# Optimization experiments

Measured on AMD Instinct MI355X. Metric: run time of the kernel, lower is better.

The kernel has to match this reference:

```python
import jax, jax.numpy as jnp
import numpy as np

N = 8192
HEADS = 2
IN_F = 256
OUT_F = 64
NEG_SLOPE = 0.2
ADJ_DENSITY = 0.01


def setup_inputs() -> dict:
    key = jax.random.key(0)
    k1, k2, k3, k4, k5 = jax.random.split(key, 5)
    x = jax.random.normal(k1, (N, IN_F), dtype=jnp.float32)
    # xavier_uniform with relu gain sqrt(2)
    def xavier(k, shape, fan_in, fan_out):
        gain = float(np.sqrt(2.0))
        limit = gain * float(np.sqrt(6.0 / (fan_in + fan_out)))
        return jax.random.uniform(k, shape, jnp.float32, -limit, limit)
    W = xavier(k2, (HEADS, IN_F, OUT_F), IN_F, OUT_F)
    a_src = xavier(k3, (HEADS, OUT_F, 1), OUT_F, 1)
    a_dst = xavier(k4, (HEADS, OUT_F, 1), OUT_F, 1)
    bias = jnp.zeros((HEADS * OUT_F,), dtype=jnp.float32)
    # sparse 0/1 adjacency used purely as a mask
    adj = (jax.random.uniform(k5, (N, N)) < ADJ_DENSITY).astype(jnp.float32)
    return {"x": x, "W": W, "a_src": a_src, "a_dst": a_dst, "bias": bias, "adj": adj}


def reference(x, W, a_src, a_dst, bias, adj):
    n = x.shape[0]
    # h: (H, N, out)
    h = jnp.einsum('ni,hio->hno', x, W)
    # additive attention logits: e[h,i,j] = src[h,i] + dst[h,j]
    s = jnp.einsum('hno,ho->hn', h, a_src[..., 0])  # (H, N)
    d = jnp.einsum('hno,ho->hn', h, a_dst[..., 0])  # (H, N)
    e = jax.nn.leaky_relu(s[:, :, None] + d[:, None, :], negative_slope=NEG_SLOPE)
    # mask: disallowed where adj + I == 0 (self-loops always kept)
    mask = (adj + jnp.eye(n, dtype=adj.dtype)) == 0  # (N, N)
    e = jnp.where(mask[None], -jnp.inf, e)
    alpha = jax.nn.softmax(e, axis=-1)  # (H, N, N); dropout p=0 -> identity
    out = jnp.einsum('hnm,hmo->hno', alpha, h)  # (H, N, out)
    # concat heads -> (N, H*out), then bias
    out = out.transpose(1, 0, 2).reshape(n, -1) + bias
    return out
```

## Files before the change

kernel.cpp:

```cpp
#include <hip/hip_runtime.h>
#include <hip/hip_bf16.h>
#include <math.h>

#define NN 8192
#define IN_F 256
#define OUT_F 64
#define HEADS 2
#define NEG_SLOPE 0.2f
#define QS 160

__device__ __forceinline__ float lrelu(float v) { return v > 0.0f ? v : NEG_SLOPE * v; }
__device__ __forceinline__ float bf_lo(unsigned u) { return __uint_as_float(u << 16); }
__device__ __forceinline__ float bf_hi(unsigned u) { return __uint_as_float(u & 0xffff0000u); }

__global__ __launch_bounds__(256) void gat_proj(
    const float* __restrict__ x, const float* __restrict__ W,
    const float* __restrict__ a_src, const float* __restrict__ a_dst,
    __hip_bfloat16* __restrict__ hb, float* __restrict__ s_arr,
    float2* __restrict__ d2)
{
    __shared__ float  xs[16 * IN_F];
    __shared__ float2 wch[32 * 64];
    const int tid = threadIdx.x;
    const int r0 = blockIdx.x * 16;

    {
        const float4* xg = (const float4*)(x + (size_t)r0 * IN_F);
        float4* xs4 = (float4*)xs;
#pragma unroll
        for (int v = 0; v < 4; ++v) xs4[v * 256 + tid] = xg[v * 256 + tid];
    }

    const int wave = tid >> 6;
    const int lane = tid & 63;
    const int rbase = wave * 4;

    const float* __restrict__ W0 = W;
    const float* __restrict__ W1 = W + IN_F * OUT_F;

    float acc[4][2] = {{0.f,0.f},{0.f,0.f},{0.f,0.f},{0.f,0.f}};

    for (int kc = 0; kc < 8; ++kc) {
        __syncthreads();
#pragma unroll
        for (int t = 0; t < 8; ++t) {
            const int idx = t * 256 + tid;
            const int kk = idx >> 6, c = idx & 63;
            wch[idx] = make_float2(W0[(kc * 32 + kk) * 64 + c],
                                   W1[(kc * 32 + kk) * 64 + c]);
        }
        __syncthreads();
#pragma unroll 8
        for (int kk = 0; kk < 32; ++kk) {
            const float2 wv = wch[kk * 64 + lane];
#pragma unroll
            for (int r = 0; r < 4; ++r) {
                const float xv = xs[(rbase + r) * IN_F + kc * 32 + kk];
                acc[r][0] += xv * wv.x;
                acc[r][1] += xv * wv.y;
            }
        }
    }

    const float as0 = a_src[lane],         ad0 = a_dst[lane];
    const float as1 = a_src[OUT_F + lane], ad1 = a_dst[OUT_F + lane];

#pragma unroll
    for (int r = 0; r < 4; ++r) {
        const int row = r0 + rbase + r;
        hb[(size_t)row * 128 + lane]      = __float2bfloat16(acc[r][0]);
        hb[(size_t)row * 128 + 64 + lane] = __float2bfloat16(acc[r][1]);
        float v0 = acc[r][0] * as0;
        float v1 = acc[r][0] * ad0;
        float v2 = acc[r][1] * as1;
        float v3 = acc[r][1] * ad1;
#pragma unroll
        for (int off = 32; off; off >>= 1) {
            v0 += __shfl_xor(v0, off);
            v1 += __shfl_xor(v1, off);
            v2 += __shfl_xor(v2, off);
            v3 += __shfl_xor(v3, off);
        }
        if (lane == 0) {
            s_arr[row]      = v0;
            s_arr[NN + row] = v2;
            d2[row] = make_float2(v1, v3);
        }
    }
}

__global__ __launch_bounds__(256, 4) void gat_scan_agg(
    const float* __restrict__ adj, const __hip_bfloat16* __restrict__ hb,
    const float* __restrict__ s_arr, const float2* __restrict__ d2,
    const float* __restrict__ bias, float* __restrict__ out)
{
    __shared__ ushort qs[4][QS];
    __shared__ float2 qw[4][QS];
    const int wave = threadIdx.x >> 6;
    const int lane = threadIdx.x & 63;
    const int i = blockIdx.x * 4 + wave;

    const float s0 = s_arr[i], s1 = s_arr[NN + i];
    const float2 di = d2[i];
    const float M0 = lrelu(s0 + di.x);
    const float M1 = lrelu(s1 + di.y);

    const uint4* __restrict__ arow = (const uint4*)(adj + (size_t)i * NN);
    uint accs[4];
#pragma unroll
    for (int g = 0; g < 4; ++g) {
        uint acc = 0;
#pragma unroll
        for (int b = 0; b < 8; ++b) {
            const uint4 a = arow[(g * 8 + b) * 64 + lane];
            const uint nib = ((a.x >> 23) & 1u) | ((a.y >> 22) & 2u) |
                             ((a.z >> 21) & 4u) | ((a.w >> 20) & 8u);
            acc |= nib << (4 * b);
        }
        accs[g] = acc;
    }

    if (lane == ((i & 255) >> 2)) {
        const int c = i >> 8;
        const int g = c >> 3;
        const uint m = ~(1u << (((c & 7) << 2) | (i & 3)));
        accs[g] &= m;
    }

    const int mycnt = __popc(accs[0]) + __popc(accs[1]) + __popc(accs[2]) + __popc(accs[3]);
    int pre = mycnt;
#pragma unroll
    for (int off = 1; off < 64; off <<= 1) {
        const int v = __shfl_up(pre, off);
        if (lane >= off) pre += v;
    }
    const int base0 = 1 + pre - mycnt;
    int cnt = 1 + __shfl(pre, 63);

    if (lane == 0) qs[wave][0] = (ushort)i;
    {
        int slot = base0;
#pragma unroll
        for (int g = 0; g < 4; ++g) {
            uint w = accs[g];
            while (w) {
                const int idx = __builtin_ctz(w);
                w &= w - 1;
                const int j = g * 2048 + ((idx >> 2) << 8) + (lane << 2) + (idx & 3);
                if (slot < QS - 8) qs[wave][slot] = (ushort)j;
                ++slot;
            }
        }
    }
    cnt = min(cnt, QS - 8);
    if (lane < 7) qs[wave][cnt + lane] = (ushort)i;

    float l0 = 0.f, l1 = 0.f;
    for (int e = lane; e < cnt; e += 64) {
        const int j = qs[wave][e];
        const float2 dv = d2[j];
        const float w0 = __expf(lrelu(s0 + dv.x) - M0);
        const float w1 = __expf(lrelu(s1 + dv.y) - M1);
        qw[wave][e] = make_float2(w0, w1);
        l0 += w0;
        l1 += w1;
    }
    if (lane < 7) qw[wave][cnt + lane] = make_float2(0.f, 0.f);
#pragma unroll
    for (int off = 32; off; off >>= 1) {
        l0 += __shfl_xor(l0, off);
        l1 += __shfl_xor(l1, off);
    }

    const int g = lane >> 4, gl = lane & 15;
    const bool head0 = (gl < 8);
    const uint4* __restrict__ hb4 = (const uint4*)hb;
    float acc[8] = {0.f,0.f,0.f,0.f,0.f,0.f,0.f,0.f};

    const int cntp = (cnt + 7) & ~7;
    for (int e = 0; e < cntp; e += 8) {
        const int ja = qs[wave][e + g];
        const int jb = qs[wave][e + 4 + g];
        const float2 wa2 = qw[wave][e + g];
        const float2 wb2 = qw[wave][e + 4 + g];
        const float wa = head0 ? wa2.x : wa2.y;
        const float wb = head0 ? wb2.x : wb2.y;
        const uint4 va = hb4[(size_t)ja * 16 + gl];
        const uint4 vb = hb4[(size_t)jb * 16 + gl];
        acc[0] += wa * bf_lo(va.x) + wb * bf_lo(vb.x);
        acc[1] += wa * bf_hi(va.x) + wb * bf_hi(vb.x);
        acc[2] += wa * bf_lo(va.y) + wb * bf_lo(vb.y);
        acc[3] += wa * bf_hi(va.y) + wb * bf_hi(vb.y);
        acc[4] += wa * bf_lo(va.z) + wb * bf_lo(vb.z);
        acc[5] += wa * bf_hi(va.z) + wb * bf_hi(vb.z);
        acc[6] += wa * bf_lo(va.w) + wb * bf_lo(vb.w);
        acc[7] += wa * bf_hi(va.w) + wb * bf_hi(vb.w);
    }

#pragma unroll
    for (int off = 16; off <= 32; off <<= 1) {
#pragma unroll
        for (int k = 0; k < 8; ++k) acc[k] += __shfl_xor(acc[k], off);
    }

    const float inv0 = 1.0f / l0;
    const float inv1 = 1.0f / l1;
    if (lane < 16) {
        const float inv = head0 ? inv0 : inv1;
        float4 r0, r1;
        const float4 b0 = *(const float4*)(bias + gl * 8);
        const float4 b1 = *(const float4*)(bias + gl * 8 + 4);
        r0.x = acc[0] * inv + b0.x; r0.y = acc[1] * inv + b0.y;
        r0.z = acc[2] * inv + b0.z; r0.w = acc[3] * inv + b0.w;
        r1.x = acc[4] * inv + b1.x; r1.y = acc[5] * inv + b1.y;
        r1.z = acc[6] * inv + b1.z; r1.w = acc[7] * inv + b1.w;
        float4* orow = (float4*)(out + (size_t)i * 128);
        orow[gl * 2]     = r0;
        orow[gl * 2 + 1] = r1;
    }
}

extern "C" void kernel_launch(void* const* d_in, const int* in_sizes, int n_in,
                              void* d_out, int out_size, void* d_ws, size_t ws_size,
                              hipStream_t stream) {
    const float* x     = (const float*)d_in[0];
    const float* W     = (const float*)d_in[1];
    const float* a_src = (const float*)d_in[2];
    const float* a_dst = (const float*)d_in[3];
    const float* bias  = (const float*)d_in[4];
    const float* adj   = (const float*)d_in[5];
    float* out = (float*)d_out;

    char* ws = (char*)d_ws;
    __hip_bfloat16* hb = (__hip_bfloat16*)ws;
    float*  s_arr = (float*)(ws + (size_t)2 * 1024 * 1024);
    float2* d2    = (float2*)(s_arr + (size_t)HEADS * NN);

    gat_proj<<<NN / 16, 256, 0, stream>>>(x, W, a_src, a_dst, hb, s_arr, d2);
    gat_scan_agg<<<NN / 4, 256, 0, stream>>>(adj, hb, s_arr, d2, bias, out);
}
```

Before: 76.55 us.

## Overlap adjacency bitmask scan with projection in a combined first kernel

The adjacency scan that packs the dense float mask into bits moves out of the aggregation kernel into extra blocks of the projection kernel. Those blocks write a compact bitmask to workspace. The aggregation kernel then reads 1 KB per row instead of 32 KB. The 256 MB adj read now overlaps with the projection GEMM instead of running after it, at the cost of an extra 8 MB bitmask write and read. The launch bound on the main kernel also drops its occupancy hint.

```diff
diff --git a/kernel.cpp b/kernel.cpp
--- a/kernel.cpp
+++ b/kernel.cpp
@@ -8,89 +8,116 @@
 #define HEADS 2
 #define NEG_SLOPE 0.2f
 #define QS 160
+#define PROJ_BLOCKS 512
+#define SCAN_BLOCKS (NN / 4)
 
 __device__ __forceinline__ float lrelu(float v) { return v > 0.0f ? v : NEG_SLOPE * v; }
 __device__ __forceinline__ float bf_lo(unsigned u) { return __uint_as_float(u << 16); }
 __device__ __forceinline__ float bf_hi(unsigned u) { return __uint_as_float(u & 0xffff0000u); }
 
-__global__ __launch_bounds__(256) void gat_proj(
+__global__ __launch_bounds__(256) void gat_proj_scan(
     const float* __restrict__ x, const float* __restrict__ W,
     const float* __restrict__ a_src, const float* __restrict__ a_dst,
+    const float* __restrict__ adj,
     __hip_bfloat16* __restrict__ hb, float* __restrict__ s_arr,
-    float2* __restrict__ d2)
+    float2* __restrict__ d2, uint* __restrict__ bm)
 {
     __shared__ float  xs[16 * IN_F];
     __shared__ float2 wch[32 * 64];
     const int tid = threadIdx.x;
-    const int r0 = blockIdx.x * 16;
-
-    {
-        const float4* xg = (const float4*)(x + (size_t)r0 * IN_F);
-        float4* xs4 = (float4*)xs;
-#pragma unroll
-        for (int v = 0; v < 4; ++v) xs4[v * 256 + tid] = xg[v * 256 + tid];
-    }
-
-    const int wave = tid >> 6;
-    const int lane = tid & 63;
-    const int rbase = wave * 4;
-
-    const float* __restrict__ W0 = W;
-    const float* __restrict__ W1 = W + IN_F * OUT_F;
-
-    float acc[4][2] = {{0.f,0.f},{0.f,0.f},{0.f,0.f},{0.f,0.f}};
-
-    for (int kc = 0; kc < 8; ++kc) {
-        __syncthreads();
-#pragma unroll
-        for (int t = 0; t < 8; ++t) {
-            const int idx = t * 256 + tid;
-            const int kk = idx >> 6, c = idx & 63;
-            wch[idx] = make_float2(W0[(kc * 32 + kk) * 64 + c],
-                                   W1[(kc * 32 + kk) * 64 + c]);
-        }
-        __syncthreads();
+
+    if (blockIdx.x < PROJ_BLOCKS) {
+        const int r0 = blockIdx.x * 16;
+        {
+            const float4* xg = (const float4*)(x + (size_t)r0 * IN_F);
+            float4* xs4 = (float4*)xs;
+#pragma unroll
+            for (int v = 0; v < 4; ++v) xs4[v * 256 + tid] = xg[v * 256 + tid];
+        }
+
+        const int wave = tid >> 6;
+        const int lane = tid & 63;
+        const int rbase = wave * 4;
+
+        const float* __restrict__ W0 = W;
+        const float* __restrict__ W1 = W + IN_F * OUT_F;
+
+        float acc[4][2] = {{0.f,0.f},{0.f,0.f},{0.f,0.f},{0.f,0.f}};
+
+        for (int kc = 0; kc < 8; ++kc) {
+            __syncthreads();
+#pragma unroll
+            for (int t = 0; t < 8; ++t) {
+                const int idx = t * 256 + tid;
+                const int kk = idx >> 6, c = idx & 63;
+                wch[idx] = make_float2(W0[(kc * 32 + kk) * 64 + c],
+                                       W1[(kc * 32 + kk) * 64 + c]);
+            }
+            __syncthreads();
 #pragma unroll 8
-        for (int kk = 0; kk < 32; ++kk) {
-            const float2 wv = wch[kk * 64 + lane];
-#pragma unroll
-            for (int r = 0; r < 4; ++r) {
-                const float xv = xs[(rbase + r) * IN_F + kc * 32 + kk];
-                acc[r][0] += xv * wv.x;
-                acc[r][1] += xv * wv.y;
-            }
-        }
-    }
-
-    const float as0 = a_src[lane],         ad0 = a_dst[lane];
-    const float as1 = a_src[OUT_F + lane], ad1 = a_dst[OUT_F + lane];
-
-#pragma unroll
-    for (int r = 0; r < 4; ++r) {
-        const int row = r0 + rbase + r;
-        hb[(size_t)row * 128 + lane]      = __float2bfloat16(acc[r][0]);
-        hb[(size_t)row * 128 + 64 + lane] = __float2bfloat16(acc[r][1]);
-        float v0 = acc[r][0] * as0;
-        float v1 = acc[r][0] * ad0;
-        float v2 = acc[r][1] * as1;
-        float v3 = acc[r][1] * ad1;
-#pragma unroll
-        for (int off = 32; off; off >>= 1) {
-            v0 += __shfl_xor(v0, off);
-            v1 += __shfl_xor(v1, off);
-            v2 += __shfl_xor(v2, off);
-            v3 += __shfl_xor(v3, off);
-        }
-        if (lane == 0) {
-            s_arr[row]      = v0;
-            s_arr[NN + row] = v2;
-            d2[row] = make_float2(v1, v3);
-        }
+            for (int kk = 0; kk < 32; ++kk) {
+                const float2 wv = wch[kk * 64 + lane];
+#pragma unroll
+                for (int r = 0; r < 4; ++r) {
+                    const float xv = xs[(rbase + r) * IN_F + kc * 32 + kk];
+                    acc[r][0] += xv * wv.x;
+                    acc[r][1] += xv * wv.y;
+                }
+            }
+        }
+
+        const float as0 = a_src[lane],         ad0 = a_dst[lane];
+        const float as1 = a_src[OUT_F + lane], ad1 = a_dst[OUT_F + lane];
+
+#pragma unroll
+        for (int r = 0; r < 4; ++r) {
+            const int row = r0 + rbase + r;
+            hb[(size_t)row * 128 + lane]      = __float2bfloat16(acc[r][0]);
+            hb[(size_t)row * 128 + 64 + lane] = __float2bfloat16(acc[r][1]);
+            float v0 = acc[r][0] * as0;
+            float v1 = acc[r][0] * ad0;
+            float v2 = acc[r][1] * as1;
+            float v3 = acc[r][1] * ad1;
+#pragma unroll
+            for (int off = 32; off; off >>= 1) {
+                v0 += __shfl_xor(v0, off);
+                v1 += __shfl_xor(v1, off);
+                v2 += __shfl_xor(v2, off);
+                v3 += __shfl_xor(v3, off);
+            }
+            if (lane == 0) {
+                s_arr[row]      = v0;
+                s_arr[NN + row] = v2;
+                d2[row] = make_float2(v1, v3);
+            }
+        }
+    } else {
+        const int sb = blockIdx.x - PROJ_BLOCKS;
+        const int wave = tid >> 6;
+        const int lane = tid & 63;
+        const int i = sb * 4 + wave;
+
+        const uint4* __restrict__ arow = (const uint4*)(adj + (size_t)i * NN);
+        uint accs[4];
+
+#pragma unroll
+        for (int g = 0; g < 4; ++g) {
+            uint acc = 0;
+#pragma unroll
+            for (int b = 0; b < 8; ++b) {
+                const uint4 a = arow[(g * 8 + b) * 64 + lane];
+                const uint nib = ((a.x >> 23) & 1u) | ((a.y >> 22) & 2u) |
+                                 ((a.z >> 21) & 4u) | ((a.w >> 20) & 8u);
+                acc |= nib << (4 * b);
+            }
+            accs[g] = acc;
+        }
+        ((uint4*)(bm + (size_t)i * 256))[lane] = make_uint4(accs[0], accs[1], accs[2], accs[3]);
     }
 }
 
-__global__ __launch_bounds__(256, 4) void gat_scan_agg(
-    const float* __restrict__ adj, const __hip_bfloat16* __restrict__ hb,
+__global__ __launch_bounds__(256) void gat_main(
+    const uint* __restrict__ bm, const __hip_bfloat16* __restrict__ hb,
     const float* __restrict__ s_arr, const float2* __restrict__ d2,
     const float* __restrict__ bias, float* __restrict__ out)
 {
@@ -105,29 +132,15 @@
     const float M0 = lrelu(s0 + di.x);
     const float M1 = lrelu(s1 + di.y);
 
-    const uint4* __restrict__ arow = (const uint4*)(adj + (size_t)i * NN);
-    uint accs[4];
-#pragma unroll
-    for (int g = 0; g < 4; ++g) {
-        uint acc = 0;
-#pragma unroll
-        for (int b = 0; b < 8; ++b) {
-            const uint4 a = arow[(g * 8 + b) * 64 + lane];
-            const uint nib = ((a.x >> 23) & 1u) | ((a.y >> 22) & 2u) |
-                             ((a.z >> 21) & 4u) | ((a.w >> 20) & 8u);
-            acc |= nib << (4 * b);
-        }
-        accs[g] = acc;
-    }
-
+    uint4 w4 = ((const uint4*)(bm + (size_t)i * 256))[lane];
     if (lane == ((i & 255) >> 2)) {
         const int c = i >> 8;
         const int g = c >> 3;
         const uint m = ~(1u << (((c & 7) << 2) | (i & 3)));
-        accs[g] &= m;
-    }
-
-    const int mycnt = __popc(accs[0]) + __popc(accs[1]) + __popc(accs[2]) + __popc(accs[3]);
+        if (g == 0) w4.x &= m; else if (g == 1) w4.y &= m;
+        else if (g == 2) w4.z &= m; else w4.w &= m;
+    }
+    const int mycnt = __popc(w4.x) + __popc(w4.y) + __popc(w4.z) + __popc(w4.w);
     int pre = mycnt;
 #pragma unroll
     for (int off = 1; off < 64; off <<= 1) {
@@ -139,10 +152,11 @@
 
     if (lane == 0) qs[wave][0] = (ushort)i;
     {
+        uint words[4] = {w4.x, w4.y, w4.z, w4.w};
         int slot = base0;
 #pragma unroll
         for (int g = 0; g < 4; ++g) {
-            uint w = accs[g];
+            uint w = words[g];
             while (w) {
                 const int idx = __builtin_ctz(w);
                 w &= w - 1;
@@ -235,7 +249,9 @@
     __hip_bfloat16* hb = (__hip_bfloat16*)ws;
     float*  s_arr = (float*)(ws + (size_t)2 * 1024 * 1024);
     float2* d2    = (float2*)(s_arr + (size_t)HEADS * NN);
-
-    gat_proj<<<NN / 16, 256, 0, stream>>>(x, W, a_src, a_dst, hb, s_arr, d2);
-    gat_scan_agg<<<NN / 4, 256, 0, stream>>>(adj, hb, s_arr, d2, bias, out);
+    uint*   bm    = (uint*)(d2 + NN);
+
+    gat_proj_scan<<<PROJ_BLOCKS + SCAN_BLOCKS, 256, 0, stream>>>(
+        x, W, a_src, a_dst, adj, hb, s_arr, d2, bm);
+    gat_main<<<NN / 4, 256, 0, stream>>>(bm, hb, s_arr, d2, bias, out);
 }
```

Result: faster. 63.21 us (-17.4%).
